# Kernel optimization log

Measured on AMD Instinct MI355X. Metric: run time of the kernel, lower is better.

The kernel has to match this reference:

```python
import jax, jax.numpy as jnp
import numpy as np

# dims: p replicas, b batch, s seq, d hidden, H heads, HK kv heads, DH head_dim
P, B, S, D = 4, 2, 2048, 2048
H, HK, DH = 16, 4, 128
G = H // HK  # GQA groups


def setup_inputs() -> dict:
    key = jax.random.key(0)
    ks = jax.random.split(key, 11)
    w = 0.02
    return {
        "hidden_states": jax.random.normal(ks[0], (P * B, S, D), jnp.float32),
        "cos": jax.random.uniform(ks[1], (B, P, DH), jnp.float32, -1.0, 1.0),
        "sin": jax.random.uniform(ks[2], (B, P, DH), jnp.float32, -1.0, 1.0),
        "Wq": jax.random.normal(ks[3], (D, H * DH), jnp.float32) * w,
        "bq": jnp.zeros((H * DH,), jnp.float32),
        "Wk": jax.random.normal(ks[4], (D, HK * DH), jnp.float32) * w,
        "bk": jnp.zeros((HK * DH,), jnp.float32),
        "Wv": jax.random.normal(ks[5], (D, HK * DH), jnp.float32) * w,
        "bv": jnp.zeros((HK * DH,), jnp.float32),
        "Wo": jax.random.normal(ks[6], (H * DH, D), jnp.float32) * w,
    }


def _rotate_half(x):
    x1, x2 = jnp.split(x, 2, axis=-1)
    return jnp.concatenate((-x2, x1), axis=-1)


def reference(hidden_states, cos, sin, Wq, bq, Wk, bk, Wv, bv, Wo):
    # projections: (p*b, s, h*dh)
    q = hidden_states @ Wq + bq
    k = hidden_states @ Wk + bk
    v = hidden_states @ Wv + bv

    def to_bshpd(x, h):  # '(p b) s (h d_h) -> b s h p d_h'
        return x.reshape(P, B, S, h, DH).transpose(1, 2, 3, 0, 4)

    q = to_bshpd(q, H)   # (b, s, H, p, dh)
    k = to_bshpd(k, HK)  # (b, s, HK, p, dh)
    v = to_bshpd(v, HK)

    # replica RoPE: cos/sin (b, p, dh) broadcast over s and heads
    cos_e = cos[:, None, None, :, :]
    sin_e = sin[:, None, None, :, :]
    q = q * cos_e + _rotate_half(q) * sin_e
    k = k * cos_e + _rotate_half(k) * sin_e

    # GQA repeat: 'b s h p d -> b s (g h) p d' (group-major)
    k = jnp.tile(k, (1, 1, G, 1, 1))
    v = jnp.tile(v, (1, 1, G, 1, 1))

    # attention over the tiny replica axis p (non-causal, no dropout at eval)
    scores = jnp.einsum('bshpd,bshqd->bshpq', q, k) * (DH ** -0.5)
    attn = jax.nn.softmax(scores, axis=-1)
    o = jnp.einsum('bshpq,bshqd->bshpd', attn, v)  # (b, s, H, p, dh)

    # 'b s h p d_h -> (p b) s (h d_h)'
    o = o.transpose(3, 0, 1, 2, 4).reshape(P * B, S, H * DH)
    return o @ Wo
```

## Files before the change

kernel.cpp:

```cpp
#include <hip/hip_runtime.h>
#include <stdint.h>

typedef unsigned short u16;
typedef __bf16 bf16x8 __attribute__((ext_vector_type(8)));
typedef float f32x4 __attribute__((ext_vector_type(4)));
typedef uint32_t u32x4 __attribute__((ext_vector_type(4)));

constexpr int P_  = 4, B_ = 2, S_ = 2048, D_ = 2048;
constexpr int H_  = 16, HK_ = 4, DH_ = 128;
constexpr int M_  = P_ * B_ * S_;
constexpr int NQKV = (H_ + 2 * HK_) * DH_;
constexpr int K_  = D_;

__device__ __forceinline__ float bf2f(u16 u) {
  union { unsigned int i; float f; } v; v.i = ((unsigned int)u) << 16; return v.f;
}
__device__ __forceinline__ u16 f2bf(float f) {
  union { float f; unsigned int i; } v; v.f = f;
  unsigned int r = v.i + 0x7fffu + ((v.i >> 16) & 1u);
  return (u16)(r >> 16);
}
__device__ __forceinline__ uint32_t pkbf(float lo, float hi) {
  return (uint32_t)f2bf(lo) | ((uint32_t)f2bf(hi) << 16);
}

__device__ __forceinline__ void gll16(const u16* g, u16* l) {
  __builtin_amdgcn_global_load_lds(
      (const __attribute__((address_space(1))) uint32_t*)g,
      (__attribute__((address_space(3))) uint32_t*)l, 16, 0, 0);
}

__global__ __launch_bounds__(256) void transpose_f32_bf16(
    const float* __restrict__ src, u16* __restrict__ dst,
    int rows, int cols, size_t dstOff, int ld) {
  __shared__ float tile[32][33];
  int c0 = blockIdx.x * 32, r0 = blockIdx.y * 32;
  int tx = threadIdx.x, ty = threadIdx.y;
#pragma unroll
  for (int i = 0; i < 32; i += 8)
    tile[ty + i][tx] = src[(size_t)(r0 + ty + i) * cols + (c0 + tx)];
  __syncthreads();
#pragma unroll
  for (int i = 0; i < 32; i += 8)
    dst[dstOff + (size_t)(c0 + ty + i) * ld + (r0 + tx)] = f2bf(tile[tx][ty + i]);
}

__global__ __launch_bounds__(256) void f32_to_bf16(
    const float* __restrict__ src, u16* __restrict__ dst, size_t n8) {
  size_t i = (size_t)blockIdx.x * 256 + threadIdx.x;
  size_t stride = (size_t)gridDim.x * 256;
  for (; i < n8; i += stride) {
    f32x4 a = ((const f32x4*)src)[2 * i];
    f32x4 b = ((const f32x4*)src)[2 * i + 1];
    u32x4 o = (u32x4){pkbf(a[0], a[1]), pkbf(a[2], a[3]),
                      pkbf(b[0], b[1]), pkbf(b[2], b[3])};
    ((u32x4*)dst)[i] = o;
  }
}

__global__ void build_bias(const float* __restrict__ bq, const float* __restrict__ bk,
                           const float* __restrict__ bv, float* __restrict__ bias) {
  int n = blockIdx.x * 256 + threadIdx.x;
  if (n < NQKV)
    bias[n] = (n < H_ * DH_) ? bq[n]
            : (n < H_ * DH_ + HK_ * DH_) ? bk[n - H_ * DH_]
            : bv[n - H_ * DH_ - HK_ * DH_];
}

#define MM16(AF, BF, I0)                                                      \
  {                                                                           \
    _Pragma("unroll") for (int i = 0; i < 4; i++) {                           \
      _Pragma("unroll") for (int j = 0; j < 4; j++) {                         \
        acc[(I0) + i][j] = __builtin_amdgcn_mfma_f32_16x16x32_bf16(           \
            AF[(I0) + i], BF[j], acc[(I0) + i][j], 0, 0, 0);                  \
      }                                                                       \
    }                                                                         \
  }

template <bool OUTF32>
__global__ __launch_bounds__(512, 2) void gemm8(
    const u16* __restrict__ A, int lda, const u16* __restrict__ BT,
    void* __restrict__ Cv, int N, int K, const float* __restrict__ bias,
    int nbx) {
  extern __shared__ u16 Ls[];

  const int tid  = threadIdx.x;
  const int wid  = tid >> 6;
  const int lane = tid & 63;
  const int wm = wid >> 2, wn = wid & 3;
  const int tm = lane & 15, quad = lane >> 4;

  const int nwg = gridDim.x;
  const int q = nwg >> 3, r = nwg & 7;
  const int xcd = blockIdx.x & 7, lin = blockIdx.x >> 3;
  const int wg = (xcd < r ? xcd * (q + 1) : r * (q + 1) + (xcd - r) * q) + lin;
  const int bx = wg % nbx, by = wg / nbx;
  const int mBase = by * 256, nBase = bx * 256;

  const int sRow  = tid >> 3;
  const int chunk = (tid & 7) ^ (sRow & 7);
  const u16* aSt = A  + (size_t)(mBase + sRow) * lda + chunk * 8;
  const u16* bSt = BT + (size_t)(nBase + sRow) * (size_t)K + chunk * 8;

  const int off0 = tm * 64 + ((quad)     ^ (tm & 7)) * 8;
  const int off1 = tm * 64 + ((quad ^ 4) ^ (tm & 7)) * 8;

  f32x4 acc[8][4];
#pragma unroll
  for (int i = 0; i < 8; i++)
#pragma unroll
    for (int j = 0; j < 4; j++) acc[i][j] = (f32x4){0.f, 0.f, 0.f, 0.f};

  const int nt = K >> 6;

  auto stA = [&](int tile, int half) {
    const u16* s0 = aSt + (size_t)(half * 128) * lda + tile * 64;
    u16* d = Ls + (((tile & 1) * 2 + 0) * 2 + half) * 8192 + wid * 512;
    gll16(s0, d);
    gll16(s0 + (size_t)64 * lda, d + 4096);
  };
  auto stB = [&](int tile, int half) {
    const u16* s0 = bSt + (size_t)(half * 128) * (size_t)K + tile * 64;
    u16* d = Ls + (((tile & 1) * 2 + 1) * 2 + half) * 8192 + wid * 512;
    gll16(s0, d);
    gll16(s0 + (size_t)64 * K, d + 4096);
  };

  stA(0, 0); stA(0, 1); stB(0, 0); stB(0, 1);
  stA(1, 0); stA(1, 1);
  asm volatile("s_waitcnt vmcnt(4)" ::: "memory");
  __builtin_amdgcn_s_barrier();

  for (int t = 0; t < nt; ++t) {
    const int s = t & 1;
    const u16* aH = Ls + ((s * 2 + 0) * 2 + wm) * 8192;
    const u16* bH = Ls + ((s * 2 + 1) * 2 + (wn >> 1)) * 8192 + (wn & 1) * 4096;
    bf16x8 af0[8], bf0[4], af1[8], bf1[4];

#pragma unroll
    for (int i = 0; i < 4; i++) af0[i] = *(const bf16x8*)(aH + i * 1024 + off0);
#pragma unroll
    for (int j = 0; j < 4; j++) bf0[j] = *(const bf16x8*)(bH + j * 1024 + off0);
    if (t + 1 < nt) stB(t + 1, 0);
    __builtin_amdgcn_s_barrier();
    asm volatile("s_waitcnt lgkmcnt(0)" ::: "memory");
    __builtin_amdgcn_sched_barrier(0);
    __builtin_amdgcn_s_setprio(1);
    MM16(af0, bf0, 0);
    __builtin_amdgcn_s_setprio(0);
    __builtin_amdgcn_s_barrier();

#pragma unroll
    for (int i = 4; i < 8; i++) af0[i] = *(const bf16x8*)(aH + i * 1024 + off0);
#pragma unroll
    for (int i = 0; i < 4; i++) af1[i] = *(const bf16x8*)(aH + i * 1024 + off1);
    if (t + 1 < nt) stB(t + 1, 1);
    __builtin_amdgcn_s_barrier();
    asm volatile("s_waitcnt lgkmcnt(0)" ::: "memory");
    __builtin_amdgcn_sched_barrier(0);
    __builtin_amdgcn_s_setprio(1);
    MM16(af0, bf0, 4);
    __builtin_amdgcn_s_setprio(0);
    __builtin_amdgcn_s_barrier();

#pragma unroll
    for (int i = 4; i < 8; i++) af1[i] = *(const bf16x8*)(aH + i * 1024 + off1);
#pragma unroll
    for (int j = 0; j < 4; j++) bf1[j] = *(const bf16x8*)(bH + j * 1024 + off1);
    __builtin_amdgcn_s_barrier();
    asm volatile("s_waitcnt lgkmcnt(0)" ::: "memory");
    __builtin_amdgcn_sched_barrier(0);
    __builtin_amdgcn_s_setprio(1);
    MM16(af1, bf1, 0);
    __builtin_amdgcn_s_setprio(0);
    __builtin_amdgcn_s_barrier();

    if (t + 2 < nt) { stA(t + 2, 0); stA(t + 2, 1); }
    __builtin_amdgcn_s_barrier();
    __builtin_amdgcn_s_setprio(1);
    MM16(af1, bf1, 4);
    __builtin_amdgcn_s_setprio(0);
    if (t + 2 < nt) {
      asm volatile("s_waitcnt vmcnt(4)" ::: "memory");
    } else {
      asm volatile("s_waitcnt vmcnt(0)" ::: "memory");
    }
    __builtin_amdgcn_s_barrier();
  }

  float bi[4] = {0.f, 0.f, 0.f, 0.f};
  if (bias != nullptr) {
#pragma unroll
    for (int j = 0; j < 4; j++) bi[j] = bias[nBase + wn * 64 + j * 16 + tm];
  }
#pragma unroll
  for (int i = 0; i < 8; i++) {
    const int row0 = mBase + wm * 128 + i * 16 + quad * 4;
#pragma unroll
    for (int j = 0; j < 4; j++) {
      const int col = nBase + wn * 64 + j * 16 + tm;
#pragma unroll
      for (int rr = 0; rr < 4; rr++) {
        float v = acc[i][j][rr] + bi[j];
        if (OUTF32)
          ((float*)Cv)[(size_t)(row0 + rr) * N + col] = v;
        else
          ((u16*)Cv)[(size_t)(row0 + rr) * N + col] = f2bf(v);
      }
    }
  }
}

template <bool AF32, bool OUTF32>
__global__ __launch_bounds__(256) void gemm_bt(
    const void* __restrict__ Av, int lda, const u16* __restrict__ BT,
    void* __restrict__ Cv, int N, int K, const float* __restrict__ bias) {
  __shared__ __align__(16) u16 As[128 * 32];
  __shared__ __align__(16) u16 Bs[128 * 32];

  const int tid  = threadIdx.x;
  const int wave = tid >> 6;
  const int lane = tid & 63;
  const int waveM = wave & 1, waveN = wave >> 1;

  const int mBase = blockIdx.y * 128;
  const int nBase = blockIdx.x * 128;

  const int l4 = lane >> 2;
  const int cg = (lane & 3) ^ ((lane >> 3) & 3);

  const float* agf0 = nullptr; const float* agf1 = nullptr;
  const u16*   agh0 = nullptr; const u16*   agh1 = nullptr;
  if (AF32) {
    agf0 = (const float*)Av + (size_t)(mBase + wave * 16 + l4) * lda + cg * 8;
    agf1 = agf0 + (size_t)64 * lda;
  } else {
    agh0 = (const u16*)Av + (size_t)(mBase + wave * 16 + l4) * lda + cg * 8;
    agh1 = agh0 + (size_t)64 * lda;
  }
  const u16* bg0 = BT + (size_t)(nBase + wave * 16 + l4) * K + cg * 8;
  const u16* bg1 = bg0 + (size_t)64 * K;
  u16* al0 = As + wave * 512 + lane * 8;
  u16* al1 = As + 2048 + wave * 512 + lane * 8;
  u16* bl0 = Bs + wave * 512 + lane * 8;
  u16* bl1 = Bs + 2048 + wave * 512 + lane * 8;

  const int tm = lane & 15;
  const int quad = lane >> 4;
  const int rslot = quad ^ ((tm >> 1) & 3);
  const u16* aRead = As + (waveM * 64 + tm) * 32 + rslot * 8;
  const u16* bRead = Bs + (waveN * 64 + tm) * 32 + rslot * 8;

  f32x4 acc[4][4];
#pragma unroll
  for (int i = 0; i < 4; i++)
#pragma unroll
    for (int j = 0; j < 4; j++) acc[i][j] = (f32x4){0.f, 0.f, 0.f, 0.f};

  for (int k0 = 0; k0 < K; k0 += 32) {
    u32x4 ra0, ra1;
    if (AF32) {
      f32x4 lo0 = *(const f32x4*)(agf0 + k0);
      f32x4 hi0 = *(const f32x4*)(agf0 + k0 + 4);
      f32x4 lo1 = *(const f32x4*)(agf1 + k0);
      f32x4 hi1 = *(const f32x4*)(agf1 + k0 + 4);
      ra0 = (u32x4){pkbf(lo0[0], lo0[1]), pkbf(lo0[2], lo0[3]),
                    pkbf(hi0[0], hi0[1]), pkbf(hi0[2], hi0[3])};
      ra1 = (u32x4){pkbf(lo1[0], lo1[1]), pkbf(lo1[2], lo1[3]),
                    pkbf(hi1[0], hi1[1]), pkbf(hi1[2], hi1[3])};
    } else {
      ra0 = *(const u32x4*)(agh0 + k0);
      ra1 = *(const u32x4*)(agh1 + k0);
    }
    u32x4 rb0 = *(const u32x4*)(bg0 + k0);
    u32x4 rb1 = *(const u32x4*)(bg1 + k0);
    __syncthreads();
    *(u32x4*)al0 = ra0;
    *(u32x4*)al1 = ra1;
    *(u32x4*)bl0 = rb0;
    *(u32x4*)bl1 = rb1;
    __syncthreads();

    bf16x8 af[4], bf[4];
#pragma unroll
    for (int i = 0; i < 4; i++) {
      af[i] = *(const bf16x8*)(aRead + i * 512);
      bf[i] = *(const bf16x8*)(bRead + i * 512);
    }
#pragma unroll
    for (int i = 0; i < 4; i++)
#pragma unroll
      for (int j = 0; j < 4; j++)
        acc[i][j] = __builtin_amdgcn_mfma_f32_16x16x32_bf16(af[i], bf[j], acc[i][j], 0, 0, 0);
  }

  float bi[4] = {0.f, 0.f, 0.f, 0.f};
  if (bias != nullptr) {
#pragma unroll
    for (int j = 0; j < 4; j++) bi[j] = bias[nBase + waveN * 64 + j * 16 + tm];
  }
#pragma unroll
  for (int i = 0; i < 4; i++) {
    int row0 = mBase + waveM * 64 + i * 16 + quad * 4;
#pragma unroll
    for (int j = 0; j < 4; j++) {
      int col = nBase + waveN * 64 + j * 16 + tm;
#pragma unroll
      for (int r = 0; r < 4; r++) {
        float v = acc[i][j][r] + bi[j];
        if (OUTF32)
          ((float*)Cv)[(size_t)(row0 + r) * N + col] = v;
        else
          ((u16*)Cv)[(size_t)(row0 + r) * N + col] = f2bf(v);
      }
    }
  }
}

__global__ __launch_bounds__(64) void attn_xreplica(
    u16* __restrict__ QKV, const float* __restrict__ cosb,
    const float* __restrict__ sinb) {
  const int blk = blockIdx.x;
  const int s  = blk & (S_ - 1);
  const int hk = (blk >> 11) & (HK_ - 1);
  const int b  = blk >> 13;
  const int t  = threadIdx.x;
  const int d0 = t, d1 = t + 64;

  u16* rp[P_];
  float kr[P_][2], vv[P_][2], cs[P_][2], sn[P_][2];
#pragma unroll
  for (int p = 0; p < P_; p++) {
    rp[p] = QKV + ((size_t)((p * B_ + b) * S_ + s)) * NQKV;
    float c0 = cosb[(b * P_ + p) * DH_ + d0];
    float c1 = cosb[(b * P_ + p) * DH_ + d1];
    float s0 = sinb[(b * P_ + p) * DH_ + d0];
    float s1 = sinb[(b * P_ + p) * DH_ + d1];
    cs[p][0] = c0; cs[p][1] = c1; sn[p][0] = s0; sn[p][1] = s1;
    float k0 = bf2f(rp[p][H_ * DH_ + hk * DH_ + d0]);
    float k1 = bf2f(rp[p][H_ * DH_ + hk * DH_ + d1]);
    kr[p][0] = k0 * c0 - k1 * s0;
    kr[p][1] = k1 * c1 + k0 * s1;
    vv[p][0] = bf2f(rp[p][(H_ + HK_) * DH_ + hk * DH_ + d0]);
    vv[p][1] = bf2f(rp[p][(H_ + HK_) * DH_ + hk * DH_ + d1]);
  }

  const float scale = 0.08838834764831845f;
#pragma unroll
  for (int hi = 0; hi < 4; hi++) {
    const int h = hk + hi * HK_;
    float qr[P_][2];
#pragma unroll
    for (int p = 0; p < P_; p++) {
      float q0 = bf2f(rp[p][h * DH_ + d0]);
      float q1 = bf2f(rp[p][h * DH_ + d1]);
      qr[p][0] = q0 * cs[p][0] - q1 * sn[p][0];
      qr[p][1] = q1 * cs[p][1] + q0 * sn[p][1];
    }
    float sc[P_][P_];
#pragma unroll
    for (int pq = 0; pq < P_; pq++)
#pragma unroll
      for (int pk = 0; pk < P_; pk++) {
        float v = qr[pq][0] * kr[pk][0] + qr[pq][1] * kr[pk][1];
#pragma unroll
        for (int off = 32; off >= 1; off >>= 1) v += __shfl_xor(v, off, 64);
        sc[pq][pk] = v;
      }
#pragma unroll
    for (int pq = 0; pq < P_; pq++) {
      float x0 = sc[pq][0] * scale, x1 = sc[pq][1] * scale;
      float x2 = sc[pq][2] * scale, x3 = sc[pq][3] * scale;
      float m = fmaxf(fmaxf(x0, x1), fmaxf(x2, x3));
      float e0 = __expf(x0 - m), e1 = __expf(x1 - m);
      float e2 = __expf(x2 - m), e3 = __expf(x3 - m);
      float inv = 1.0f / (e0 + e1 + e2 + e3);
      float w0 = e0 * inv, w1 = e1 * inv, w2 = e2 * inv, w3 = e3 * inv;
      float o0 = w0 * vv[0][0] + w1 * vv[1][0] + w2 * vv[2][0] + w3 * vv[3][0];
      float o1 = w0 * vv[0][1] + w1 * vv[1][1] + w2 * vv[2][1] + w3 * vv[3][1];
      u16* orow = rp[pq] + h * DH_;
      orow[d0] = f2bf(o0);
      orow[d1] = f2bf(o1);
    }
  }
}

extern "C" void kernel_launch(void* const* d_in, const int* in_sizes, int n_in,
                              void* d_out, int out_size, void* d_ws, size_t ws_size,
                              hipStream_t stream) {
  const float* hs   = (const float*)d_in[0];
  const float* cosb = (const float*)d_in[1];
  const float* sinb = (const float*)d_in[2];
  const float* Wq   = (const float*)d_in[3];
  const float* bq   = (const float*)d_in[4];
  const float* Wk   = (const float*)d_in[5];
  const float* bk   = (const float*)d_in[6];
  const float* Wv   = (const float*)d_in[7];
  const float* bv   = (const float*)d_in[8];
  const float* Wo   = (const float*)d_in[9];

  u16*   WqkvT = (u16*)d_ws;
  u16*   WoT   = WqkvT + (size_t)NQKV * K_;
  float* biasQ = (float*)(WoT + (size_t)D_ * K_);
  u16*   QKV   = (u16*)(biasQ + 4096);
  u16*   hsb   = QKV + (size_t)M_ * NQKV;
  const size_t need = (size_t)((char*)(hsb + (size_t)M_ * D_) - (char*)d_ws);

  dim3 tb(32, 8);
  transpose_f32_bf16<<<dim3(64, 64), tb, 0, stream>>>(Wq, WqkvT, D_, H_ * DH_, 0, K_);
  transpose_f32_bf16<<<dim3(16, 64), tb, 0, stream>>>(Wk, WqkvT, D_, HK_ * DH_,
                                                      (size_t)(H_ * DH_) * K_, K_);
  transpose_f32_bf16<<<dim3(16, 64), tb, 0, stream>>>(Wv, WqkvT, D_, HK_ * DH_,
                                                      (size_t)((H_ + HK_) * DH_) * K_, K_);
  transpose_f32_bf16<<<dim3(64, 64), tb, 0, stream>>>(Wo, WoT, H_ * DH_, D_, 0, K_);
  build_bias<<<12, 256, 0, stream>>>(bq, bk, bv, biasQ);

  if (ws_size >= need) {
    static int attrSet = 0;
    if (!attrSet) {
      hipFuncSetAttribute((const void*)gemm8<false>,
                          hipFuncAttributeMaxDynamicSharedMemorySize, 131072);
      hipFuncSetAttribute((const void*)gemm8<true>,
                          hipFuncAttributeMaxDynamicSharedMemorySize, 131072);
      attrSet = 1;
    }
    f32_to_bf16<<<2048, 256, 0, stream>>>(hs, hsb, (size_t)M_ * D_ / 8);
    gemm8<false><<<dim3((NQKV / 256) * (M_ / 256)), 512, 131072, stream>>>(
        hsb, K_, WqkvT, (void*)QKV, NQKV, K_, biasQ, NQKV / 256);
    attn_xreplica<<<B_ * HK_ * S_, 64, 0, stream>>>(QKV, cosb, sinb);
    gemm8<true><<<dim3((D_ / 256) * (M_ / 256)), 512, 131072, stream>>>(
        QKV, NQKV, WoT, d_out, D_, K_, nullptr, D_ / 256);
  } else {
    gemm_bt<true, false><<<dim3(NQKV / 128, M_ / 128), 256, 0, stream>>>(
        (const void*)hs, K_, WqkvT, (void*)QKV, NQKV, K_, biasQ);
    attn_xreplica<<<B_ * HK_ * S_, 64, 0, stream>>>(QKV, cosb, sinb);
    gemm_bt<false, true><<<dim3(D_ / 128, M_ / 128), 256, 0, stream>>>(
        (const void*)QKV, NQKV, WoT, d_out, D_, K_, nullptr);
  }
}
```

Baseline: 647.7 us.

## Software-pipeline LDS fragment loads across GEMM k-tiles with partial lgkmcnt waits

Restructures the GEMM main loop so the first A/B fragment group for the next k-tile is loaded from LDS at the end of the current iteration. Within the iteration, subsequent fragment loads are issued before the MFMA block that precedes them. Partial lgkmcnt waits replace full drains, letting LDS reads overlap MFMA execution. This aims to hide LDS latency behind matrix math, at the cost of more live registers and reliance on correct wait counts (the stB global-to-LDS loads also count toward lgkmcnt semantics).

```diff
diff --git a/kernel.cpp b/kernel.cpp
--- a/kernel.cpp
+++ b/kernel.cpp
@@ -67,12 +67,12 @@
             : bv[n - H_ * DH_ - HK_ * DH_];
 }
 
-#define MM16(AF, BF, I0)                                                      \
+#define MM16(AF, AO, BF, I0)                                                  \
   {                                                                           \
     _Pragma("unroll") for (int i = 0; i < 4; i++) {                           \
       _Pragma("unroll") for (int j = 0; j < 4; j++) {                         \
         acc[(I0) + i][j] = __builtin_amdgcn_mfma_f32_16x16x32_bf16(           \
-            AF[(I0) + i], BF[j], acc[(I0) + i][j], 0, 0, 0);                  \
+            AF[(AO) + i], BF[j], acc[(I0) + i][j], 0, 0, 0);                  \
       }                                                                       \
     }                                                                         \
   }
@@ -125,60 +125,72 @@
     gll16(s0, d);
     gll16(s0 + (size_t)64 * K, d + 4096);
   };
+  auto aHalf = [&](int s) -> const u16* {
+    return Ls + ((s * 2 + 0) * 2 + wm) * 8192;
+  };
+  auto bHalf = [&](int s) -> const u16* {
+    return Ls + ((s * 2 + 1) * 2 + (wn >> 1)) * 8192 + (wn & 1) * 4096;
+  };
 
   stA(0, 0); stA(0, 1); stB(0, 0); stB(0, 1);
   stA(1, 0); stA(1, 1);
   asm volatile("s_waitcnt vmcnt(4)" ::: "memory");
   __builtin_amdgcn_s_barrier();
 
+  bf16x8 af0lo[4], bf0[4];
+  {
+    const u16* aH = aHalf(0);
+    const u16* bH = bHalf(0);
+#pragma unroll
+    for (int i = 0; i < 4; i++) af0lo[i] = *(const bf16x8*)(aH + i * 1024 + off0);
+#pragma unroll
+    for (int j = 0; j < 4; j++) bf0[j] = *(const bf16x8*)(bH + j * 1024 + off0);
+  }
+
   for (int t = 0; t < nt; ++t) {
     const int s = t & 1;
-    const u16* aH = Ls + ((s * 2 + 0) * 2 + wm) * 8192;
-    const u16* bH = Ls + ((s * 2 + 1) * 2 + (wn >> 1)) * 8192 + (wn & 1) * 4096;
-    bf16x8 af0[8], bf0[4], af1[8], bf1[4];
-
-#pragma unroll
-    for (int i = 0; i < 4; i++) af0[i] = *(const bf16x8*)(aH + i * 1024 + off0);
-#pragma unroll
-    for (int j = 0; j < 4; j++) bf0[j] = *(const bf16x8*)(bH + j * 1024 + off0);
+    const u16* aH = aHalf(s);
+    const u16* bH = bHalf(s);
+    bf16x8 af0hi[4], af1[8], bf1[4];
+
+#pragma unroll
+    for (int i = 0; i < 4; i++)
+      af0hi[i] = *(const bf16x8*)(aH + (i + 4) * 1024 + off0);
     if (t + 1 < nt) stB(t + 1, 0);
     __builtin_amdgcn_s_barrier();
+    asm volatile("s_waitcnt lgkmcnt(4)" ::: "memory");
+    __builtin_amdgcn_sched_barrier(0);
+    __builtin_amdgcn_s_setprio(1);
+    MM16(af0lo, 0, bf0, 0);
+    __builtin_amdgcn_s_setprio(0);
+    __builtin_amdgcn_s_barrier();
+
+#pragma unroll
+    for (int i = 0; i < 8; i++)
+      af1[i] = *(const bf16x8*)(aH + i * 1024 + off1);
+#pragma unroll
+    for (int j = 0; j < 4; j++)
+      bf1[j] = *(const bf16x8*)(bH + j * 1024 + off1);
+    if (t + 1 < nt) stB(t + 1, 1);
+    __builtin_amdgcn_s_barrier();
+    asm volatile("s_waitcnt lgkmcnt(12)" ::: "memory");
+    __builtin_amdgcn_sched_barrier(0);
+    __builtin_amdgcn_s_setprio(1);
+    MM16(af0hi, 0, bf0, 4);
+    __builtin_amdgcn_s_setprio(0);
+    __builtin_amdgcn_s_barrier();
+
     asm volatile("s_waitcnt lgkmcnt(0)" ::: "memory");
     __builtin_amdgcn_sched_barrier(0);
     __builtin_amdgcn_s_setprio(1);
-    MM16(af0, bf0, 0);
+    MM16(af1, 0, bf1, 0);
     __builtin_amdgcn_s_setprio(0);
     __builtin_amdgcn_s_barrier();
 
-#pragma unroll
-    for (int i = 4; i < 8; i++) af0[i] = *(const bf16x8*)(aH + i * 1024 + off0);
-#pragma unroll
-    for (int i = 0; i < 4; i++) af1[i] = *(const bf16x8*)(aH + i * 1024 + off1);
-    if (t + 1 < nt) stB(t + 1, 1);
-    __builtin_amdgcn_s_barrier();
-    asm volatile("s_waitcnt lgkmcnt(0)" ::: "memory");
-    __builtin_amdgcn_sched_barrier(0);
+    if (t + 2 < nt) { stA(t + 2, 0); stA(t + 2, 1); }
+    __builtin_amdgcn_s_barrier();
     __builtin_amdgcn_s_setprio(1);
-    MM16(af0, bf0, 4);
-    __builtin_amdgcn_s_setprio(0);
-    __builtin_amdgcn_s_barrier();
-
-#pragma unroll
-    for (int i = 4; i < 8; i++) af1[i] = *(const bf16x8*)(aH + i * 1024 + off1);
-#pragma unroll
-    for (int j = 0; j < 4; j++) bf1[j] = *(const bf16x8*)(bH + j * 1024 + off1);
-    __builtin_amdgcn_s_barrier();
-    asm volatile("s_waitcnt lgkmcnt(0)" ::: "memory");
-    __builtin_amdgcn_sched_barrier(0);
-    __builtin_amdgcn_s_setprio(1);
-    MM16(af1, bf1, 0);
-    __builtin_amdgcn_s_setprio(0);
-    __builtin_amdgcn_s_barrier();
-
-    if (t + 2 < nt) { stA(t + 2, 0); stA(t + 2, 1); }
-    __builtin_amdgcn_s_barrier();
-    __builtin_amdgcn_s_setprio(1);
-    MM16(af1, bf1, 4);
+    MM16(af1, 4, bf1, 4);
     __builtin_amdgcn_s_setprio(0);
     if (t + 2 < nt) {
       asm volatile("s_waitcnt vmcnt(4)" ::: "memory");
@@ -186,6 +198,16 @@
       asm volatile("s_waitcnt vmcnt(0)" ::: "memory");
     }
     __builtin_amdgcn_s_barrier();
+    if (t + 1 < nt) {
+      const u16* aHn = aHalf(s ^ 1);
+      const u16* bHn = bHalf(s ^ 1);
+#pragma unroll
+      for (int i = 0; i < 4; i++)
+        af0lo[i] = *(const bf16x8*)(aHn + i * 1024 + off0);
+#pragma unroll
+      for (int j = 0; j < 4; j++)
+        bf0[j] = *(const bf16x8*)(bHn + j * 1024 + off0);
+    }
   }
 
   float bi[4] = {0.f, 0.f, 0.f, 0.f};
```

Result: no change. 650.7 us (+0.4%).
